# Kernel tuning notes

Measured on AMD Instinct MI355X. Metric: run time of the kernel, lower is better.

## Reference

```python
import jax, jax.numpy as jnp
import numpy as np

H, D, BS = 32, 128, 64          # num_heads, head_dim, gate block_size
GATE_DIM = 64
GATE_TEMP = 2.0                 # _GATE_TARGET_TEMPERATURE
CLAMP_MIN, CLAMP_MAX = -50.0, 50.0


def _rotate_half(x):
    x1, x2 = jnp.split(x, 2, axis=-1)
    return jnp.concatenate([-x2, x1], axis=-1)


def setup_inputs() -> dict:
    key = jax.random.key(0)
    ks = jax.random.split(key, 8)
    B, S, E = 1, 2048, 4096
    hidden_states = jax.random.normal(ks[0], (B, S, E), jnp.float32) * 0.02
    # standard RoPE tables, [B, S, D]
    inv_freq = 1.0 / (10000.0 ** (jnp.arange(0, D, 2, dtype=jnp.float32) / D))
    freqs = jnp.arange(S, dtype=jnp.float32)[:, None] * inv_freq[None, :]
    emb = jnp.concatenate([freqs, freqs], axis=-1)
    cos = jnp.broadcast_to(jnp.cos(emb)[None], (B, S, D)).astype(jnp.float32)
    sin = jnp.broadcast_to(jnp.sin(emb)[None], (B, S, D)).astype(jnp.float32)
    Wq = jax.random.normal(ks[1], (E, E), jnp.float32) * 0.02
    Wk = jax.random.normal(ks[2], (E, E), jnp.float32) * 0.02
    Wv = jax.random.normal(ks[3], (E, E), jnp.float32) * 0.02
    Wo = jax.random.normal(ks[4], (E, E), jnp.float32) * 0.02
    Wg_q = jax.random.normal(ks[5], (GATE_DIM, D), jnp.float32) * 0.05
    Wg_k = jax.random.normal(ks[6], (GATE_DIM, D), jnp.float32) * 0.05
    return {"hidden_states": hidden_states, "cos": cos, "sin": sin,
            "Wq": Wq, "Wk": Wk, "Wv": Wv, "Wo": Wo,
            "Wg_q": Wg_q, "Wg_k": Wg_k}


def reference(hidden_states, cos, sin, Wq, Wk, Wv, Wo, Wg_q, Wg_k):
    B, S, E = hidden_states.shape
    scale = np.float32(1.0 / np.sqrt(D))

    # ---- base attention (training path: full dense attention w/ scores) ----
    q = (hidden_states @ Wq.T).reshape(B, S, H, D).transpose(0, 2, 1, 3)  # [B,H,S,D]
    k = (hidden_states @ Wk.T).reshape(B, S, H, D).transpose(0, 2, 1, 3)
    v = (hidden_states @ Wv.T).reshape(B, S, H, D).transpose(0, 2, 1, 3)

    # _apply_rotary_pos_emb: cos/sin are 3D [B,S,D] -> unsqueeze head dim
    c, s = cos[:, None], sin[:, None]
    q = q * c + _rotate_half(q) * s
    k = k * c + _rotate_half(k) * s

    scores = jnp.einsum('bhqd,bhkd->bhqk', q, k) * scale  # [B,H,S,S]
    causal = jnp.tril(jnp.ones((S, S), dtype=bool))
    scores = jnp.where(causal, scores, -jnp.inf)
    attn = jax.nn.softmax(scores, axis=-1)
    ctx = jnp.einsum('bhqk,bhkd->bhqd', attn, v)
    attn_output = ctx.transpose(0, 2, 1, 3).reshape(B, S, E) @ Wo.T

    # ---- _compute_gate_target: blockwise maxpool -> clamp -> tempered softmax ----
    NB = S // BS  # S divisible by BS, so the -inf padding branch is a no-op
    block_max = scores.reshape(B, H, NB, BS, NB, BS).max(axis=(3, 5))  # [B,H,NB,NB]
    finite = jnp.isfinite(block_max)
    block_max = jnp.where(finite, jnp.clip(block_max, CLAMP_MIN, CLAMP_MAX), block_max)
    gate_target = jax.nn.softmax(
        block_max.reshape(B, H, NB * NB) / GATE_TEMP, axis=-1
    ).reshape(B, H, NB, NB)

    # ---- AttnGate prediction: mean-pooled block Q/K -> low-rank block logits ----
    qb = q.reshape(B, H, NB, BS, D).mean(axis=3)  # [B,H,NB,D]
    kb = k.reshape(B, H, NB, BS, D).mean(axis=3)
    gq = jnp.einsum('bhnd,gd->bhng', qb, Wg_q)
    gk = jnp.einsum('bhnd,gd->bhng', kb, Wg_k)
    glogits = jnp.einsum('bhqg,bhkg->bhqk', gq, gk) * np.float32(1.0 / np.sqrt(GATE_DIM))
    bmask = jnp.tril(jnp.ones((NB, NB), dtype=bool))  # block-causal
    glogits = jnp.where(bmask, glogits, -jnp.inf)
    gate_pred = jax.nn.softmax(
        glogits.reshape(B, H, NB * NB), axis=-1
    ).reshape(B, H, NB, NB)

    return attn_output, gate_pred, gate_target
```

## Files before the change

kernel.cpp:

```cpp
#include <hip/hip_runtime.h>
#include <stdint.h>

#define S_LEN 2048
#define EMB   4096
#define NHEAD 32
#define DHEAD 128
#define NBLK  32
#define GDIM  64

typedef float  f32x4  __attribute__((ext_vector_type(4)));
typedef __bf16 bf16x8 __attribute__((ext_vector_type(8)));
typedef unsigned short u16;

__device__ __forceinline__ u16 f2bf(float f) {
  uint32_t u = __float_as_uint(f);
  u += 0x7fffu + ((u >> 16) & 1u);
  return (u16)(u >> 16);
}
__device__ __forceinline__ float bf2f(u16 u) {
  return __uint_as_float(((uint32_t)u) << 16);
}

__device__ __forceinline__ void ld_lds16(const u16* g, u16* l) {
  __builtin_amdgcn_global_load_lds((const __attribute__((address_space(1))) void*)g,
                                   (__attribute__((address_space(3))) void*)l, 16, 0, 0);
}

__global__ void conv_f32_bf16(const float* __restrict__ in, u16* __restrict__ out, int n4) {
  int i = blockIdx.x * 256 + threadIdx.x;
  if (i >= n4) return;
  float4 v = ((const float4*)in)[i];
  ushort4 o;
  o.x = f2bf(v.x); o.y = f2bf(v.y); o.z = f2bf(v.z); o.w = f2bf(v.w);
  ((ushort4*)out)[i] = o;
}

__global__ void conv3_f32_bf16(const float* __restrict__ a, const float* __restrict__ b,
                               const float* __restrict__ c, u16* __restrict__ oa,
                               u16* __restrict__ ob, u16* __restrict__ oc, int n4) {
  int i = blockIdx.x * 256 + threadIdx.x;
  if (i >= n4) return;
  const float* in = (blockIdx.y == 0) ? a : (blockIdx.y == 1) ? b : c;
  u16* out = (blockIdx.y == 0) ? oa : (blockIdx.y == 1) ? ob : oc;
  float4 v = ((const float4*)in)[i];
  ushort4 o;
  o.x = f2bf(v.x); o.y = f2bf(v.y); o.z = f2bf(v.z); o.w = f2bf(v.w);
  ((ushort4*)out)[i] = o;
}

__global__ void __launch_bounds__(512, 2) qkv_gemm_256(
    const u16* __restrict__ A, const u16* __restrict__ Bq, const u16* __restrict__ Bk,
    const u16* __restrict__ Bv, u16* __restrict__ outq, u16* __restrict__ outk,
    u16* __restrict__ outvt, const float* __restrict__ cosp, const float* __restrict__ sinp)
{
  extern __shared__ u16 lds[];

  const int tid  = threadIdx.x;
  const int w    = tid >> 6;
  const int lane = tid & 63;
  const int r    = lane & 15;
  const int qd   = lane >> 4;
  const int wr   = w >> 2;
  const int wc   = w & 3;

  const int which = blockIdx.x >> 4;
  const int nt    = blockIdx.x & 15;
  const int m0    = blockIdx.y * 256;
  const int n0    = nt * 256;
  const int K     = EMB;
  const u16* B = (which == 0) ? Bq : (which == 1) ? Bk : Bv;

  const int cb0 = (wc >> 1) * 128 + (wc & 1) * 32;
  const int cb1 = cb0 + 16;
  const int cb2 = cb0 + 64;
  const int cb3 = cb0 + 80;

  const int fragoff = r * 32 + ((qd ^ ((r >> 1) & 3)) << 3);

  const int srow_st = w * 16 + (lane >> 2);
  const int sslot   = ((lane & 3) ^ ((lane >> 3) & 3)) * 8;
  const u16* Ab0 = A + (size_t)(m0 + srow_st) * K + sslot;
  const u16* Ab1 = Ab0 + (size_t)128 * K;
  const u16* Bb0 = B + (size_t)(n0 + srow_st) * K + sslot;
  const u16* Bb1 = Bb0 + (size_t)128 * K;

  f32x4 acc[8][4];
#pragma unroll
  for (int mi = 0; mi < 8; ++mi)
#pragma unroll
    for (int ni = 0; ni < 4; ++ni) acc[mi][ni] = (f32x4){0.f, 0.f, 0.f, 0.f};

  auto stageA = [&](int tt) {
    u16* d = lds + (tt & 3) * 8192 + w * 512;
    const int kk = tt * 32;
    ld_lds16(Ab0 + kk, d);
    ld_lds16(Ab1 + kk, d + 4096);
  };
  auto stageB = [&](int tt) {
    u16* d = lds + 32768 + (tt & 3) * 8192 + w * 512;
    const int kk = tt * 32;
    ld_lds16(Bb0 + kk, d);
    ld_lds16(Bb1 + kk, d + 4096);
  };

  stageA(0); stageB(0);
  stageA(1); stageB(1);
  stageA(2); stageB(2);

  for (int t = 0; t < 128; ++t) {
    const int buf = t & 3;
    if (t < 126)       asm volatile("s_waitcnt vmcnt(8) lgkmcnt(0)" ::: "memory");
    else if (t == 126) asm volatile("s_waitcnt vmcnt(4) lgkmcnt(0)" ::: "memory");
    else               asm volatile("s_waitcnt vmcnt(0) lgkmcnt(0)" ::: "memory");
    __builtin_amdgcn_sched_barrier(0);
    __builtin_amdgcn_s_barrier();

    const u16* lAb = lds + buf * 8192 + wr * 128 * 32;
    const u16* lBb = lds + 32768 + buf * 8192;

    bf16x8 bfr[4];
    bfr[0] = *(const bf16x8*)(lBb + cb0 * 32 + fragoff);
    bfr[1] = *(const bf16x8*)(lBb + cb1 * 32 + fragoff);
    bfr[2] = *(const bf16x8*)(lBb + cb2 * 32 + fragoff);
    bfr[3] = *(const bf16x8*)(lBb + cb3 * 32 + fragoff);

    bf16x8 af[4];
#pragma unroll
    for (int mi = 0; mi < 4; ++mi) af[mi] = *(const bf16x8*)(lAb + mi * 512 + fragoff);
    if (t < 125) stageA(t + 3);

    __builtin_amdgcn_s_setprio(1);
#pragma unroll
    for (int mi = 0; mi < 4; ++mi)
#pragma unroll
      for (int ni = 0; ni < 4; ++ni)
        acc[mi][ni] = __builtin_amdgcn_mfma_f32_16x16x32_bf16(af[mi], bfr[ni], acc[mi][ni], 0, 0, 0);
    __builtin_amdgcn_s_setprio(0);

    bf16x8 af2[4];
#pragma unroll
    for (int mi = 0; mi < 4; ++mi) af2[mi] = *(const bf16x8*)(lAb + (mi + 4) * 512 + fragoff);
    if (t < 125) stageB(t + 3);

    __builtin_amdgcn_s_setprio(1);
#pragma unroll
    for (int mi = 0; mi < 4; ++mi)
#pragma unroll
      for (int ni = 0; ni < 4; ++ni)
        acc[mi + 4][ni] = __builtin_amdgcn_mfma_f32_16x16x32_bf16(af2[mi], bfr[ni], acc[mi + 4][ni], 0, 0, 0);
    __builtin_amdgcn_s_setprio(0);
  }

  if (which < 2) {
    u16* out = which ? outk : outq;
    const int hh = 2 * nt + (wc >> 1);
    const int dbase = (wc & 1) * 32;
#pragma unroll
    for (int mi = 0; mi < 8; ++mi)
#pragma unroll
      for (int ni = 0; ni < 2; ++ni) {
        const int dlo = dbase + ni * 16 + r;
#pragma unroll
        for (int rg = 0; rg < 4; ++rg) {
          int srow = m0 + wr * 128 + mi * 16 + qd * 4 + rg;
          float c = cosp[srow * DHEAD + dlo];
          float s = sinp[srow * DHEAD + dlo];
          float lo = acc[mi][ni][rg], hi = acc[mi][ni + 2][rg];
          size_t base = ((size_t)hh * S_LEN + srow) * DHEAD;
          out[base + dlo]      = f2bf(lo * c - hi * s);
          out[base + dlo + 64] = f2bf(hi * c + lo * s);
        }
      }
  } else {
    u16* lT = lds;
#pragma unroll
    for (int ch = 0; ch < 2; ++ch) {
      __syncthreads();
      if (wr == ch) {
#pragma unroll
        for (int mi = 0; mi < 8; ++mi) {
          const int lr = mi * 16 + qd * 4;
          const int cbs[4] = {cb0, cb1, cb2, cb3};
#pragma unroll
          for (int ni = 0; ni < 4; ++ni) {
            const int col = cbs[ni] + r;
#pragma unroll
            for (int rg = 0; rg < 4; ++rg)
              lT[col * 136 + lr + rg] = f2bf(acc[mi][ni][rg]);
          }
        }
      }
      __syncthreads();
      const int c = tid >> 1, sh = (tid & 1) * 64;
      const int hh2 = 2 * nt + (c >> 7), d = c & 127;
      size_t obase = ((size_t)hh2 * DHEAD + d) * S_LEN + m0 + ch * 128 + sh;
#pragma unroll
      for (int i8 = 0; i8 < 8; ++i8) {
        uint4 v = *(const uint4*)&lT[c * 136 + sh + i8 * 8];
        *(uint4*)&outvt[obase + i8 * 8] = v;
      }
    }
  }
}

__global__ void __launch_bounds__(256, 2) gemm_out(
    const u16* __restrict__ A, const u16* __restrict__ B, float* __restrict__ out)
{
  __shared__ u16 lA[128 * 32];
  __shared__ u16 lB[128 * 32];
  const int tid = threadIdx.x;
  const int w = tid >> 6, lane = tid & 63;
  const int r = lane & 15, qd = lane >> 4;
  const int m0 = blockIdx.y * 128, n0 = blockIdx.x * 128;
  const int K = EMB;

  f32x4 acc[2][8];
#pragma unroll
  for (int mi = 0; mi < 2; ++mi)
#pragma unroll
    for (int ni = 0; ni < 8; ++ni) acc[mi][ni] = (f32x4){0.f, 0.f, 0.f, 0.f};

  const u16* Ab = A + (size_t)(m0 + w * 16 + (lane >> 2)) * K + (lane & 3) * 8;
  const u16* Bb = B + (size_t)(n0 + w * 16 + (lane >> 2)) * K + (lane & 3) * 8;
  u16* lAb = &lA[(w * 16) * 32];
  u16* lBb = &lB[(w * 16) * 32];

  for (int k0 = 0; k0 < K; k0 += 32) {
    __syncthreads();
    ld_lds16(Ab + k0, lAb);
    ld_lds16(Ab + (size_t)64 * K + k0, lAb + 64 * 32);
    ld_lds16(Bb + k0, lBb);
    ld_lds16(Bb + (size_t)64 * K + k0, lBb + 64 * 32);
    __syncthreads();
    bf16x8 af0 = *(const bf16x8*)&lA[(w * 32 + r) * 32 + qd * 8];
    bf16x8 af1 = *(const bf16x8*)&lA[(w * 32 + 16 + r) * 32 + qd * 8];
#pragma unroll
    for (int ni = 0; ni < 8; ++ni) {
      bf16x8 bf = *(const bf16x8*)&lB[(ni * 16 + r) * 32 + qd * 8];
      acc[0][ni] = __builtin_amdgcn_mfma_f32_16x16x32_bf16(af0, bf, acc[0][ni], 0, 0, 0);
      acc[1][ni] = __builtin_amdgcn_mfma_f32_16x16x32_bf16(af1, bf, acc[1][ni], 0, 0, 0);
    }
  }
#pragma unroll
  for (int mi = 0; mi < 2; ++mi)
#pragma unroll
    for (int ni = 0; ni < 8; ++ni)
#pragma unroll
      for (int rg = 0; rg < 4; ++rg) {
        int srow = m0 + w * 32 + mi * 16 + qd * 4 + rg;
        out[(size_t)srow * EMB + n0 + ni * 16 + r] = acc[mi][ni][rg];
      }
}

__global__ void __launch_bounds__(256, 2) attn_fwd(
    const u16* __restrict__ qg, const u16* __restrict__ kg, const u16* __restrict__ vtg,
    u16* __restrict__ ctx, float* __restrict__ bmax)
{
  __shared__ u16 lK[64 * 132];
  __shared__ u16 lV[128 * 76];
  __shared__ u16 lP[64 * 76];
  __shared__ float lBM[4 * NBLK];

  const int tid = threadIdx.x;
  const int w = tid >> 6, lane = tid & 63;
  const int r = lane & 15, qd = lane >> 4;
  const int h = blockIdx.y;
  const u16* ksrc = kg + (size_t)h * S_LEN * DHEAD;
  const u16* vsrc = vtg + (size_t)h * DHEAD * S_LEN;
  const float scale = 0.08838834764831845f;

  for (int qsel = 0; qsel < 2; ++qsel) {
    const int qb = qsel ? (31 - (int)blockIdx.x) : (int)blockIdx.x;

    bf16x8 qf[4];
    {
      const u16* qp = qg + ((size_t)h * S_LEN + qb * 64 + w * 16 + r) * DHEAD + qd * 8;
#pragma unroll
      for (int ki = 0; ki < 4; ++ki) qf[ki] = *(const bf16x8*)(qp + ki * 32);
    }

    f32x4 o[8];
#pragma unroll
    for (int dt = 0; dt < 8; ++dt) o[dt] = (f32x4){0.f, 0.f, 0.f, 0.f};
    float m_run[4], l_run[4];
#pragma unroll
    for (int rg = 0; rg < 4; ++rg) { m_run[rg] = -__builtin_inff(); l_run[rg] = 0.f; }

    for (int kb = 0; kb <= qb; ++kb) {
      __syncthreads();
#pragma unroll
      for (int i = 0; i < 4; ++i) {
        int c = tid + 256 * i;
        int row = c >> 4, col = (c & 15) * 8;
        *(uint4*)&lK[row * 132 + col] = *(const uint4*)(ksrc + (size_t)(kb * 64 + row) * DHEAD + col);
      }
#pragma unroll
      for (int i = 0; i < 4; ++i) {
        int c = tid + 256 * i;
        int row = c >> 3, col = (c & 7) * 8;
        *(uint4*)&lV[row * 76 + col] = *(const uint4*)(vsrc + (size_t)row * S_LEN + kb * 64 + col);
      }
      __syncthreads();

      f32x4 sf[4];
#pragma unroll
      for (int nt = 0; nt < 4; ++nt) sf[nt] = (f32x4){0.f, 0.f, 0.f, 0.f};
#pragma unroll
      for (int ki = 0; ki < 4; ++ki)
#pragma unroll
        for (int nt = 0; nt < 4; ++nt) {
          bf16x8 bf = *(const bf16x8*)&lK[(nt * 16 + r) * 132 + ki * 32 + qd * 8];
          sf[nt] = __builtin_amdgcn_mfma_f32_16x16x32_bf16(qf[ki], bf, sf[nt], 0, 0, 0);
        }

      float rmax[4];
#pragma unroll
      for (int rg = 0; rg < 4; ++rg) rmax[rg] = -__builtin_inff();
#pragma unroll
      for (int nt = 0; nt < 4; ++nt)
#pragma unroll
        for (int rg = 0; rg < 4; ++rg) {
          float s = sf[nt][rg] * scale;
          if (kb == qb) {
            int col = nt * 16 + r, row = w * 16 + qd * 4 + rg;
            if (col > row) s = -__builtin_inff();
          }
          sf[nt][rg] = s;
          rmax[rg] = fmaxf(rmax[rg], s);
        }
#pragma unroll
      for (int rg = 0; rg < 4; ++rg) {
        float v = rmax[rg];
        v = fmaxf(v, __shfl_xor(v, 1));
        v = fmaxf(v, __shfl_xor(v, 2));
        v = fmaxf(v, __shfl_xor(v, 4));
        v = fmaxf(v, __shfl_xor(v, 8));
        rmax[rg] = v;
      }
      {
        float v = fmaxf(fmaxf(rmax[0], rmax[1]), fmaxf(rmax[2], rmax[3]));
        v = fmaxf(v, __shfl_xor(v, 16));
        v = fmaxf(v, __shfl_xor(v, 32));
        if (lane == 0) lBM[w * NBLK + kb] = v;
      }

      float alpha[4], rsum[4];
#pragma unroll
      for (int rg = 0; rg < 4; ++rg) {
        float mn = fmaxf(m_run[rg], rmax[rg]);
        alpha[rg] = __expf(m_run[rg] - mn);
        m_run[rg] = mn;
        rsum[rg] = 0.f;
      }
#pragma unroll
      for (int nt = 0; nt < 4; ++nt)
#pragma unroll
        for (int rg = 0; rg < 4; ++rg) {
          float p = __expf(sf[nt][rg] - m_run[rg]);
          sf[nt][rg] = p;
          rsum[rg] += p;
        }
#pragma unroll
      for (int rg = 0; rg < 4; ++rg) {
        float v = rsum[rg];
        v += __shfl_xor(v, 1);
        v += __shfl_xor(v, 2);
        v += __shfl_xor(v, 4);
        v += __shfl_xor(v, 8);
        l_run[rg] = l_run[rg] * alpha[rg] + v;
      }
#pragma unroll
      for (int nt = 0; nt < 4; ++nt)
#pragma unroll
        for (int rg = 0; rg < 4; ++rg)
          lP[(w * 16 + qd * 4 + rg) * 76 + nt * 16 + r] = f2bf(sf[nt][rg]);
#pragma unroll
      for (int dt = 0; dt < 8; ++dt)
#pragma unroll
        for (int rg = 0; rg < 4; ++rg) o[dt][rg] *= alpha[rg];
      bf16x8 pa0 = *(const bf16x8*)&lP[(w * 16 + r) * 76 + qd * 8];
      bf16x8 pa1 = *(const bf16x8*)&lP[(w * 16 + r) * 76 + 32 + qd * 8];
#pragma unroll
      for (int dt = 0; dt < 8; ++dt) {
        bf16x8 bv0 = *(const bf16x8*)&lV[(dt * 16 + r) * 76 + qd * 8];
        bf16x8 bv1 = *(const bf16x8*)&lV[(dt * 16 + r) * 76 + 32 + qd * 8];
        o[dt] = __builtin_amdgcn_mfma_f32_16x16x32_bf16(pa0, bv0, o[dt], 0, 0, 0);
        o[dt] = __builtin_amdgcn_mfma_f32_16x16x32_bf16(pa1, bv1, o[dt], 0, 0, 0);
      }
    }

    float inv[4];
#pragma unroll
    for (int rg = 0; rg < 4; ++rg) inv[rg] = 1.f / l_run[rg];
#pragma unroll
    for (int dt = 0; dt < 8; ++dt)
#pragma unroll
      for (int rg = 0; rg < 4; ++rg) {
        int srow = qb * 64 + w * 16 + qd * 4 + rg;
        ctx[(size_t)srow * EMB + h * DHEAD + dt * 16 + r] = f2bf(o[dt][rg] * inv[rg]);
      }
    __syncthreads();
    if (tid <= qb) {
      float v = fmaxf(fmaxf(lBM[0 * NBLK + tid], lBM[1 * NBLK + tid]),
                      fmaxf(lBM[2 * NBLK + tid], lBM[3 * NBLK + tid]));
      bmax[((size_t)h * NBLK + qb) * NBLK + tid] = v;
    }
  }
}

__global__ void bmean2(const u16* __restrict__ q, const u16* __restrict__ k,
                       float* __restrict__ qo, float* __restrict__ ko) {
  int nb = blockIdx.x, h = blockIdx.y, t = threadIdx.x;
  const u16* x = blockIdx.z ? k : q;
  float* out = blockIdx.z ? ko : qo;
  const u16* p = x + ((size_t)h * S_LEN + nb * 64) * DHEAD + t * 2;
  float s0 = 0.f, s1 = 0.f;
#pragma unroll 8
  for (int i = 0; i < 64; ++i) {
    uint32_t v = *(const uint32_t*)(p + (size_t)i * DHEAD);
    s0 += bf2f((u16)v);
    s1 += bf2f((u16)(v >> 16));
  }
  float2 rr = {s0 * (1.f / 64.f), s1 * (1.f / 64.f)};
  *(float2*)&out[((size_t)h * NBLK + nb) * DHEAD + t * 2] = rr;
}

__global__ void __launch_bounds__(256) gate_kernel(
    const float* __restrict__ qm, const float* __restrict__ km,
    const float* __restrict__ Wgq, const float* __restrict__ Wgk,
    const float* __restrict__ bmx, float* __restrict__ gpred, float* __restrict__ gtgt)
{
  __shared__ float gq[NBLK * GDIM], gk[NBLK * GDIM];
  __shared__ float red[256];
  const int h = blockIdx.x, tid = threadIdx.x;

  for (int i = 0; i < 8; ++i) {
    int e = tid + 256 * i;
    int n = e >> 6, g = e & 63;
    const float* qrow = qm + ((size_t)h * NBLK + n) * DHEAD;
    const float* krow = km + ((size_t)h * NBLK + n) * DHEAD;
    const float* wq = Wgq + g * DHEAD;
    const float* wk = Wgk + g * DHEAD;
    float s1 = 0.f, s2 = 0.f;
    for (int d = 0; d < DHEAD; ++d) { s1 += qrow[d] * wq[d]; s2 += krow[d] * wk[d]; }
    gq[e] = s1; gk[e] = s2;
  }
  __syncthreads();

  float gl[4];
  for (int i = 0; i < 4; ++i) {
    int idx = tid + 256 * i;
    int qn = idx >> 5, kn = idx & 31;
    if (kn <= qn) {
      float s = 0.f;
      for (int g = 0; g < GDIM; ++g) s += gq[qn * GDIM + g] * gk[kn * GDIM + g];
      gl[i] = s * 0.125f;
    } else gl[i] = -__builtin_inff();
  }
  float mx = fmaxf(fmaxf(gl[0], gl[1]), fmaxf(gl[2], gl[3]));
  red[tid] = mx; __syncthreads();
  for (int st = 128; st > 0; st >>= 1) { if (tid < st) red[tid] = fmaxf(red[tid], red[tid + st]); __syncthreads(); }
  float gmax = red[0]; __syncthreads();
  float ex[4], lsum = 0.f;
  for (int i = 0; i < 4; ++i) { ex[i] = __expf(gl[i] - gmax); lsum += ex[i]; }
  red[tid] = lsum; __syncthreads();
  for (int st = 128; st > 0; st >>= 1) { if (tid < st) red[tid] += red[tid + st]; __syncthreads(); }
  float invs = 1.f / red[0]; __syncthreads();
  for (int i = 0; i < 4; ++i) gpred[(size_t)h * 1024 + tid + 256 * i] = ex[i] * invs;

  float tl[4];
  for (int i = 0; i < 4; ++i) {
    int idx = tid + 256 * i;
    int qn = idx >> 5, kn = idx & 31;
    tl[i] = (kn <= qn) ? fminf(fmaxf(bmx[(size_t)h * 1024 + idx], -50.f), 50.f) * 0.5f
                       : -__builtin_inff();
  }
  float mx2 = fmaxf(fmaxf(tl[0], tl[1]), fmaxf(tl[2], tl[3]));
  red[tid] = mx2; __syncthreads();
  for (int st = 128; st > 0; st >>= 1) { if (tid < st) red[tid] = fmaxf(red[tid], red[tid + st]); __syncthreads(); }
  float tmax = red[0]; __syncthreads();
  float ex2[4], ls2 = 0.f;
  for (int i = 0; i < 4; ++i) { ex2[i] = __expf(tl[i] - tmax); ls2 += ex2[i]; }
  red[tid] = ls2; __syncthreads();
  for (int st = 128; st > 0; st >>= 1) { if (tid < st) red[tid] += red[tid + st]; __syncthreads(); }
  float inv2 = 1.f / red[0];
  for (int i = 0; i < 4; ++i) gtgt[(size_t)h * 1024 + tid + 256 * i] = ex2[i] * inv2;
}

extern "C" void kernel_launch(void* const* d_in, const int* in_sizes, int n_in,
                              void* d_out, int out_size, void* d_ws, size_t ws_size,
                              hipStream_t stream) {
  const float* hidden = (const float*)d_in[0];
  const float* cosp   = (const float*)d_in[1];
  const float* sinp   = (const float*)d_in[2];
  const float* Wq     = (const float*)d_in[3];
  const float* Wk     = (const float*)d_in[4];
  const float* Wv     = (const float*)d_in[5];
  const float* Wo     = (const float*)d_in[6];
  const float* Wgq    = (const float*)d_in[7];
  const float* Wgk    = (const float*)d_in[8];

  char* ws = (char*)d_ws;
  u16* wqb = (u16*)ws;
  u16* wkb = (u16*)(ws + 33554432);
  u16* hid = (u16*)(ws + 67108864);
  u16* qbf = (u16*)(ws + 83886080);
  u16* kbf = (u16*)(ws + 100663296);
  u16* vtb = (u16*)(ws + 117440512);
  float* bmx = (float*)(ws + 33554432);
  float* qmn = (float*)(ws + 33554432 + 131072);
  float* kmn = (float*)(ws + 33554432 + 655360);
  u16* ctx = hid;
  u16* wvb = (u16*)d_out;

  float* attn_out = (float*)d_out;
  float* gpred = attn_out + (size_t)S_LEN * EMB;
  float* gtgt  = gpred + NHEAD * NBLK * NBLK;

  conv3_f32_bf16<<<dim3(16384, 3), 256, 0, stream>>>(Wq, Wk, Wv, wqb, wkb, wvb, 4194304);
  conv_f32_bf16<<<8192, 256, 0, stream>>>(hidden, hid, 2097152);

  static bool attr_set = false;
  if (!attr_set) {
    (void)hipFuncSetAttribute((const void*)qkv_gemm_256,
                              hipFuncAttributeMaxDynamicSharedMemorySize, 131072);
    attr_set = true;
  }
  qkv_gemm_256<<<dim3(48, 8), 512, 131072, stream>>>(hid, wqb, wkb, wvb, qbf, kbf, vtb, cosp, sinp);

  conv_f32_bf16<<<16384, 256, 0, stream>>>(Wo, wqb, 4194304);

  attn_fwd<<<dim3(16, NHEAD), 256, 0, stream>>>(qbf, kbf, vtb, ctx, bmx);

  bmean2<<<dim3(NBLK, NHEAD, 2), 128, 0, stream>>>(qbf, kbf, qmn, kmn);
  gate_kernel<<<NHEAD, 256, 0, stream>>>(qmn, kmn, Wgq, Wgk, bmx, gpred, gtgt);

  gemm_out<<<dim3(32, 16), 256, 0, stream>>>(ctx, wqb, attn_out);
}
```

Before: 770.6 us.

## Restructure QKV GEMM main loop to K=64 double-buffered ping-pong with XCD remap

Rewrites the QKV GEMM main loop to use a K-step of 64 with two LDS buffers split into A and B halves. Global-to-LDS loads for the next step are interleaved between four MFMA quadrant phases, each fenced by barriers and vmcnt waits. The grid becomes 1D with a block-index remap that spreads tiles across the 8 XCDs, and gemm_out gets the same remap. The aim is fewer loop iterations, better LDS swizzling and better L2 locality per XCD, at the cost of more barriers per iteration and a shallower prefetch depth.

```diff
diff --git a/kernel.cpp b/kernel.cpp
--- a/kernel.cpp
+++ b/kernel.cpp
@@ -62,27 +62,28 @@
   const int qd   = lane >> 4;
   const int wr   = w >> 2;
   const int wc   = w & 3;
-
-  const int which = blockIdx.x >> 4;
-  const int nt    = blockIdx.x & 15;
-  const int m0    = blockIdx.y * 256;
+  const int hh   = wc >> 1;
+
+  const int bid   = blockIdx.x;
+  const int nb    = (bid & 7) * 48 + (bid >> 3);
+  const int xx    = nb % 48;
+  const int which = xx >> 4;
+  const int nt    = xx & 15;
+  const int m0    = (nb / 48) * 256;
   const int n0    = nt * 256;
   const int K     = EMB;
-  const u16* B = (which == 0) ? Bq : (which == 1) ? Bk : Bv;
-
-  const int cb0 = (wc >> 1) * 128 + (wc & 1) * 32;
-  const int cb1 = cb0 + 16;
-  const int cb2 = cb0 + 64;
-  const int cb3 = cb0 + 80;
-
-  const int fragoff = r * 32 + ((qd ^ ((r >> 1) & 3)) << 3);
-
-  const int srow_st = w * 16 + (lane >> 2);
-  const int sslot   = ((lane & 3) ^ ((lane >> 3) & 3)) * 8;
-  const u16* Ab0 = A + (size_t)(m0 + srow_st) * K + sslot;
-  const u16* Ab1 = Ab0 + (size_t)128 * K;
-  const u16* Bb0 = B + (size_t)(n0 + srow_st) * K + sslot;
-  const u16* Bb1 = Bb0 + (size_t)128 * K;
+  const u16* Bm = (which == 0) ? Bq : (which == 1) ? Bk : Bv;
+
+  const int swz0 = (qd ^ (r & 7)) * 8;
+  const int swz1 = ((4 + qd) ^ (r & 7)) * 8;
+  const int rowbaseA = (wr * 64 + r) * 64;
+  const int rowbaseB = (hh * 64 + (wc & 1) * 16 + r) * 64;
+
+  const int srw = tid >> 3;
+  const int sgs = ((tid & 7) ^ (srw & 7)) * 8;
+  const u16* pA0 = A + (size_t)(m0 + srw) * K + sgs;
+  const int fm = ((srw >> 5) & 1) * 64 + (srw & 31);
+  const u16* pB0 = Bm + (size_t)(n0 + fm) * K + sgs;
 
   f32x4 acc[8][4];
 #pragma unroll
@@ -90,104 +91,158 @@
 #pragma unroll
     for (int ni = 0; ni < 4; ++ni) acc[mi][ni] = (f32x4){0.f, 0.f, 0.f, 0.f};
 
-  auto stageA = [&](int tt) {
-    u16* d = lds + (tt & 3) * 8192 + w * 512;
-    const int kk = tt * 32;
-    ld_lds16(Ab0 + kk, d);
-    ld_lds16(Ab1 + kk, d + 4096);
+  auto stA = [&](int tt, int half) {
+    u16* d = lds + ((tt & 1) * 2 + half) * 8192 + w * 512;
+    const u16* g = pA0 + (size_t)(half * 128) * K + tt * 64;
+    ld_lds16(g, d);
+    ld_lds16(g + (size_t)64 * K, d + 4096);
   };
-  auto stageB = [&](int tt) {
-    u16* d = lds + 32768 + (tt & 3) * 8192 + w * 512;
-    const int kk = tt * 32;
-    ld_lds16(Bb0 + kk, d);
-    ld_lds16(Bb1 + kk, d + 4096);
+  auto stB = [&](int tt, int half) {
+    u16* d = lds + 32768 + ((tt & 1) * 2 + half) * 8192 + w * 512;
+    const u16* g = pB0 + (size_t)(half * 32) * K + tt * 64;
+    ld_lds16(g, d);
+    ld_lds16(g + (size_t)128 * K, d + 4096);
   };
 
-  stageA(0); stageB(0);
-  stageA(1); stageB(1);
-  stageA(2); stageB(2);
-
-  for (int t = 0; t < 128; ++t) {
-    const int buf = t & 3;
-    if (t < 126)       asm volatile("s_waitcnt vmcnt(8) lgkmcnt(0)" ::: "memory");
-    else if (t == 126) asm volatile("s_waitcnt vmcnt(4) lgkmcnt(0)" ::: "memory");
-    else               asm volatile("s_waitcnt vmcnt(0) lgkmcnt(0)" ::: "memory");
+  stA(0, 0); stB(0, 0); stB(0, 1); stA(0, 1);
+  asm volatile("s_waitcnt vmcnt(0)" ::: "memory");
+  __builtin_amdgcn_s_barrier();
+
+  for (int t = 0; t < 64; ++t) {
+    const u16* bufA = lds + (t & 1) * 16384;
+    const u16* bufB = lds + 32768 + (t & 1) * 16384;
+    bf16x8 aF[4][2], bLo[2][2], bHi[2][2];
+
+    {
+      const u16* ab = bufA + rowbaseA;
+      const u16* bb = bufB + rowbaseB;
+#pragma unroll
+      for (int mi = 0; mi < 4; ++mi) {
+        aF[mi][0] = *(const bf16x8*)(ab + mi * 1024 + swz0);
+        aF[mi][1] = *(const bf16x8*)(ab + mi * 1024 + swz1);
+      }
+#pragma unroll
+      for (int ni = 0; ni < 2; ++ni) {
+        bLo[ni][0] = *(const bf16x8*)(bb + ni * 2048 + swz0);
+        bLo[ni][1] = *(const bf16x8*)(bb + ni * 2048 + swz1);
+      }
+    }
+    if (t < 63) stA(t + 1, 0);
+    __builtin_amdgcn_s_barrier();
+    asm volatile("s_waitcnt lgkmcnt(0)" ::: "memory");
     __builtin_amdgcn_sched_barrier(0);
-    __builtin_amdgcn_s_barrier();
-
-    const u16* lAb = lds + buf * 8192 + wr * 128 * 32;
-    const u16* lBb = lds + 32768 + buf * 8192;
-
-    bf16x8 bfr[4];
-    bfr[0] = *(const bf16x8*)(lBb + cb0 * 32 + fragoff);
-    bfr[1] = *(const bf16x8*)(lBb + cb1 * 32 + fragoff);
-    bfr[2] = *(const bf16x8*)(lBb + cb2 * 32 + fragoff);
-    bfr[3] = *(const bf16x8*)(lBb + cb3 * 32 + fragoff);
-
-    bf16x8 af[4];
-#pragma unroll
-    for (int mi = 0; mi < 4; ++mi) af[mi] = *(const bf16x8*)(lAb + mi * 512 + fragoff);
-    if (t < 125) stageA(t + 3);
-
     __builtin_amdgcn_s_setprio(1);
 #pragma unroll
     for (int mi = 0; mi < 4; ++mi)
 #pragma unroll
-      for (int ni = 0; ni < 4; ++ni)
-        acc[mi][ni] = __builtin_amdgcn_mfma_f32_16x16x32_bf16(af[mi], bfr[ni], acc[mi][ni], 0, 0, 0);
+      for (int ni = 0; ni < 2; ++ni) {
+        acc[mi][ni] = __builtin_amdgcn_mfma_f32_16x16x32_bf16(aF[mi][0], bLo[ni][0], acc[mi][ni], 0, 0, 0);
+        acc[mi][ni] = __builtin_amdgcn_mfma_f32_16x16x32_bf16(aF[mi][1], bLo[ni][1], acc[mi][ni], 0, 0, 0);
+      }
     __builtin_amdgcn_s_setprio(0);
-
-    bf16x8 af2[4];
-#pragma unroll
-    for (int mi = 0; mi < 4; ++mi) af2[mi] = *(const bf16x8*)(lAb + (mi + 4) * 512 + fragoff);
-    if (t < 125) stageB(t + 3);
-
+    if (t < 63) asm volatile("s_waitcnt vmcnt(4)" ::: "memory");
+    else        asm volatile("s_waitcnt vmcnt(2)" ::: "memory");
+    __builtin_amdgcn_s_barrier();
+
+    {
+      const u16* bb = bufB + 8192 + rowbaseB;
+#pragma unroll
+      for (int ni = 0; ni < 2; ++ni) {
+        bHi[ni][0] = *(const bf16x8*)(bb + ni * 2048 + swz0);
+        bHi[ni][1] = *(const bf16x8*)(bb + ni * 2048 + swz1);
+      }
+    }
+    if (t < 63) stB(t + 1, 0);
+    __builtin_amdgcn_s_barrier();
+    asm volatile("s_waitcnt lgkmcnt(0)" ::: "memory");
+    __builtin_amdgcn_sched_barrier(0);
     __builtin_amdgcn_s_setprio(1);
 #pragma unroll
     for (int mi = 0; mi < 4; ++mi)
 #pragma unroll
-      for (int ni = 0; ni < 4; ++ni)
-        acc[mi + 4][ni] = __builtin_amdgcn_mfma_f32_16x16x32_bf16(af2[mi], bfr[ni], acc[mi + 4][ni], 0, 0, 0);
+      for (int ni = 0; ni < 2; ++ni) {
+        acc[mi][ni + 2] = __builtin_amdgcn_mfma_f32_16x16x32_bf16(aF[mi][0], bHi[ni][0], acc[mi][ni + 2], 0, 0, 0);
+        acc[mi][ni + 2] = __builtin_amdgcn_mfma_f32_16x16x32_bf16(aF[mi][1], bHi[ni][1], acc[mi][ni + 2], 0, 0, 0);
+      }
     __builtin_amdgcn_s_setprio(0);
+    if (t < 63) asm volatile("s_waitcnt vmcnt(4)" ::: "memory");
+    else        asm volatile("s_waitcnt vmcnt(0)" ::: "memory");
+    __builtin_amdgcn_s_barrier();
+
+    {
+      const u16* ab = bufA + 8192 + rowbaseA;
+#pragma unroll
+      for (int mi = 0; mi < 4; ++mi) {
+        aF[mi][0] = *(const bf16x8*)(ab + mi * 1024 + swz0);
+        aF[mi][1] = *(const bf16x8*)(ab + mi * 1024 + swz1);
+      }
+    }
+    if (t < 63) stB(t + 1, 1);
+    __builtin_amdgcn_s_barrier();
+    asm volatile("s_waitcnt lgkmcnt(0)" ::: "memory");
+    __builtin_amdgcn_sched_barrier(0);
+    __builtin_amdgcn_s_setprio(1);
+#pragma unroll
+    for (int mi = 0; mi < 4; ++mi)
+#pragma unroll
+      for (int ni = 0; ni < 2; ++ni) {
+        acc[mi + 4][ni + 2] = __builtin_amdgcn_mfma_f32_16x16x32_bf16(aF[mi][0], bHi[ni][0], acc[mi + 4][ni + 2], 0, 0, 0);
+        acc[mi + 4][ni + 2] = __builtin_amdgcn_mfma_f32_16x16x32_bf16(aF[mi][1], bHi[ni][1], acc[mi + 4][ni + 2], 0, 0, 0);
+      }
+    __builtin_amdgcn_s_setprio(0);
+    __builtin_amdgcn_s_barrier();
+
+    if (t < 63) stA(t + 1, 1);
+    __builtin_amdgcn_s_barrier();
+    __builtin_amdgcn_s_setprio(1);
+#pragma unroll
+    for (int mi = 0; mi < 4; ++mi)
+#pragma unroll
+      for (int ni = 0; ni < 2; ++ni) {
+        acc[mi + 4][ni] = __builtin_amdgcn_mfma_f32_16x16x32_bf16(aF[mi][0], bLo[ni][0], acc[mi + 4][ni], 0, 0, 0);
+        acc[mi + 4][ni] = __builtin_amdgcn_mfma_f32_16x16x32_bf16(aF[mi][1], bLo[ni][1], acc[mi + 4][ni], 0, 0, 0);
+      }
+    __builtin_amdgcn_s_setprio(0);
+    if (t < 63) asm volatile("s_waitcnt vmcnt(4)" ::: "memory");
+    __builtin_amdgcn_s_barrier();
   }
 
   if (which < 2) {
     u16* out = which ? outk : outq;
-    const int hh = 2 * nt + (wc >> 1);
-    const int dbase = (wc & 1) * 32;
-#pragma unroll
-    for (int mi = 0; mi < 8; ++mi)
-#pragma unroll
-      for (int ni = 0; ni < 2; ++ni) {
-        const int dlo = dbase + ni * 16 + r;
+    const int hh_out = 2 * nt + hh;
+#pragma unroll
+    for (int mi = 0; mi < 8; ++mi) {
+      const int rbase = m0 + (mi >> 2) * 128 + wr * 64 + (mi & 3) * 16 + qd * 4;
+#pragma unroll
+      for (int pp = 0; pp < 2; ++pp) {
+        const int dlo = pp * 32 + (wc & 1) * 16 + r;
 #pragma unroll
         for (int rg = 0; rg < 4; ++rg) {
-          int srow = m0 + wr * 128 + mi * 16 + qd * 4 + rg;
+          int srow = rbase + rg;
           float c = cosp[srow * DHEAD + dlo];
           float s = sinp[srow * DHEAD + dlo];
-          float lo = acc[mi][ni][rg], hi = acc[mi][ni + 2][rg];
-          size_t base = ((size_t)hh * S_LEN + srow) * DHEAD;
+          float lo = acc[mi][pp * 2 + 0][rg], hi = acc[mi][pp * 2 + 1][rg];
+          size_t base = ((size_t)hh_out * S_LEN + srow) * DHEAD;
           out[base + dlo]      = f2bf(lo * c - hi * s);
           out[base + dlo + 64] = f2bf(hi * c + lo * s);
         }
       }
+    }
   } else {
     u16* lT = lds;
 #pragma unroll
     for (int ch = 0; ch < 2; ++ch) {
       __syncthreads();
-      if (wr == ch) {
-#pragma unroll
-        for (int mi = 0; mi < 8; ++mi) {
-          const int lr = mi * 16 + qd * 4;
-          const int cbs[4] = {cb0, cb1, cb2, cb3};
-#pragma unroll
-          for (int ni = 0; ni < 4; ++ni) {
-            const int col = cbs[ni] + r;
-#pragma unroll
-            for (int rg = 0; rg < 4; ++rg)
-              lT[col * 136 + lr + rg] = f2bf(acc[mi][ni][rg]);
-          }
+#pragma unroll
+      for (int mq = 0; mq < 4; ++mq) {
+        const int mi = ch * 4 + mq;
+        const int lr = wr * 64 + mq * 16 + qd * 4;
+#pragma unroll
+        for (int ni = 0; ni < 4; ++ni) {
+          const int col = hh * 128 + (ni >> 1) * 32 + (wc & 1) * 16 + (ni & 1) * 64 + r;
+#pragma unroll
+          for (int rg = 0; rg < 4; ++rg)
+            lT[col * 136 + lr + rg] = f2bf(acc[mi][ni][rg]);
         }
       }
       __syncthreads();
@@ -211,7 +266,9 @@
   const int tid = threadIdx.x;
   const int w = tid >> 6, lane = tid & 63;
   const int r = lane & 15, qd = lane >> 4;
-  const int m0 = blockIdx.y * 128, n0 = blockIdx.x * 128;
+  const int bid = blockIdx.x + (blockIdx.y << 5);
+  const int nbx = (bid & 7) * 64 + (bid >> 3);
+  const int m0 = (nbx >> 5) * 128, n0 = (nbx & 31) * 128;
   const int K = EMB;
 
   f32x4 acc[2][8];
@@ -526,7 +583,7 @@
                               hipFuncAttributeMaxDynamicSharedMemorySize, 131072);
     attr_set = true;
   }
-  qkv_gemm_256<<<dim3(48, 8), 512, 131072, stream>>>(hid, wqb, wkb, wvb, qbf, kbf, vtb, cosp, sinp);
+  qkv_gemm_256<<<dim3(384), 512, 131072, stream>>>(hid, wqb, wkb, wvb, qbf, kbf, vtb, cosp, sinp);
 
   conv_f32_bf16<<<16384, 256, 0, stream>>>(Wo, wqb, 4194304);
 
```

Result: slower. 789.5 us (+2.4%).
